# Kernel optimization log

Hardware: AMD Instinct MI355X
Metric: run time of the kernel (lower is better)

The kernel has to match this reference:

```python
import jax, jax.numpy as jnp
import numpy as np

# MX microscaling spec: block_size=32 shared power-of-2 scale, int8 elements (MXINT8),
# vector (SIMD) ops rounded to bfloat16 as in microxcaling's simd_* / vec_* ops.
BLOCK = 32
BITS = 8  # int8 element format: grid step 2^(shared_exp - (BITS-2)), range [-2^(BITS-1), 2^(BITS-1)-1]


def bf16_round(x):
    # bfloat=16 rounding used by simd_split / simd_add / vec ops
    return x.astype(jnp.bfloat16).astype(jnp.float32)


def mx_quant(x):
    """MXINT8 fake-quant along last (contraction) axis with block-shared exponent.
    Straight-through estimator for gradients."""
    s = x.shape
    xb = x.reshape(s[:-1] + (s[-1] // BLOCK, BLOCK))
    amax = jnp.max(jnp.abs(xb), axis=-1, keepdims=True)
    shared_exp = jnp.floor(jnp.log2(jnp.where(amax > 0, amax, 1.0)))
    scale = jnp.exp2(shared_exp - (BITS - 2))
    q = jnp.clip(jnp.round(xb / scale), -(2.0 ** (BITS - 1)), 2.0 ** (BITS - 1) - 1) * scale
    q = jnp.where(amax > 0, q, 0.0).reshape(s)
    return x + jax.lax.stop_gradient(q - x)


def mx_linear(x, W, b):
    # quantize activations and weights to MX blocks along K, fp32 accumulate, bf16 bias-add
    y = jnp.einsum('btk,ok->bto', mx_quant(x), mx_quant(W))
    return bf16_round(y + b)


def mx_layernorm(x, w, b, eps=1e-5):
    mu = jnp.mean(x, axis=-1, keepdims=True)
    var = jnp.mean(jnp.square(x - mu), axis=-1, keepdims=True)
    return bf16_round((x - mu) * jax.lax.rsqrt(var + eps) * w + b)


def mx_gelu(x):
    # tanh-approx gelu as in microxcaling, bf16-rounded output
    c = jnp.float32(0.7978845608028654)  # sqrt(2/pi)
    return bf16_round(0.5 * x * (1.0 + jnp.tanh(c * (x + 0.044715 * x * x * x))))


def setup_inputs() -> dict:
    key = jax.random.key(0)
    ks = jax.random.split(key, 5)
    B, S, H = 2, 2048, 2048
    inputs = jax.random.normal(ks[0], (B, S, H), dtype=jnp.float32)
    ln_w = jnp.ones((H,), dtype=jnp.float32)
    ln_b = jnp.zeros((H,), dtype=jnp.float32)
    W1 = jax.random.normal(ks[1], (4 * H, H), dtype=jnp.float32) * (1.0 / np.sqrt(H))
    b1 = jnp.zeros((4 * H,), dtype=jnp.float32)
    W2 = jax.random.normal(ks[2], (H, 4 * H), dtype=jnp.float32) * (1.0 / np.sqrt(4 * H))
    b2 = jnp.zeros((H,), dtype=jnp.float32)
    return {"inputs": inputs, "ln_w": ln_w, "ln_b": ln_b, "W1": W1, "b1": b1, "W2": W2, "b2": b2}


def reference(inputs, ln_w, ln_b, W1, b1, W2, b2):
    # simd_split: bf16-rounded copies for MLP branch and residual branch
    x = bf16_round(inputs)
    residual = bf16_round(inputs)
    h = mx_layernorm(x, ln_w, ln_b)
    h = mx_linear(h, W1, b1)          # [B,S,4H]
    h = mx_gelu(h)
    h = mx_linear(h, W2, b2)          # [B,S,H]
    return bf16_round(residual + h)    # simd_add
```

## Files before the change

### kernel.cpp

```cpp
#include <hip/hip_runtime.h>

#define DEVI __device__ __forceinline__

typedef __bf16 bf16x8 __attribute__((ext_vector_type(8)));
typedef float f32x4 __attribute__((ext_vector_type(4)));

DEVI unsigned short f2bf(float f) {
  unsigned u = __float_as_uint(f);
  u = (u + 0x7FFFu + ((u >> 16) & 1u)) >> 16;
  return (unsigned short)u;
}
DEVI float bf2f(unsigned short h) { return __uint_as_float(((unsigned)h) << 16); }
DEVI float bf16r(float f) { return bf2f(f2bf(f)); }

DEVI void mx_scales(float amax, float& scale, float& inv) {
  unsigned eb = __float_as_uint(amax) & 0x7f800000u;
  scale = __uint_as_float(eb - (6u << 23));
  inv   = __uint_as_float((260u << 23) - eb);
}

DEVI unsigned short quantv(float v, float scale, float inv) {
  float qv = rintf(v * inv);
  qv = fminf(fmaxf(qv, -128.f), 127.f);
  return f2bf(qv * scale);
}

DEVI void quant8(const float* h, float amax, unsigned short* q) {
  if (amax > 0.f) {
    float scale, inv;
    mx_scales(amax, scale, inv);
#pragma unroll
    for (int k = 0; k < 8; ++k) q[k] = quantv(h[k], scale, inv);
  } else {
#pragma unroll
    for (int k = 0; k < 8; ++k) q[k] = 0;
  }
}

template <int N>
DEVI float qmax_step(float x) {
  int y = __builtin_amdgcn_update_dpp(0, __float_as_int(x), 0x120 | N, 0xF, 0xF, true);
  return fmaxf(x, __int_as_float(y));
}
DEVI float quad_row_max(float x) {
  x = qmax_step<1>(x);
  x = qmax_step<2>(x);
  x = qmax_step<4>(x);
  x = qmax_step<8>(x);
  return x;
}

DEVI void gl2lds16(const void* g, void* l) {
  __builtin_amdgcn_global_load_lds(
      (__attribute__((address_space(1))) void*)const_cast<void*>(g),
      (__attribute__((address_space(3))) void*)l, 16, 0, 0);
}

DEVI uint4 pack8(const unsigned short* q) {
  uint4 o;
  o.x = (unsigned)q[0] | ((unsigned)q[1] << 16);
  o.y = (unsigned)q[2] | ((unsigned)q[3] << 16);
  o.z = (unsigned)q[4] | ((unsigned)q[5] << 16);
  o.w = (unsigned)q[6] | ((unsigned)q[7] << 16);
  return o;
}

__global__ __launch_bounds__(256) void prep_k(const float* __restrict__ W1,
                                              const float* __restrict__ W2,
                                              const float* __restrict__ X,
                                              const float* __restrict__ lw,
                                              const float* __restrict__ lb,
                                              unsigned short* __restrict__ qW1,
                                              unsigned short* __restrict__ qW2,
                                              unsigned short* __restrict__ a1) {
  __shared__ float red[4];
  const int bid = blockIdx.x;
  const int t = threadIdx.x;
  if (bid < 16384) {
    const float* src = (bid < 8192) ? W1 : W2;
    unsigned short* dst = (bid < 8192) ? qW1 : qW2;
    size_t idx = (size_t)(bid & 8191) * 256 + t;
    float4 v0 = ((const float4*)src)[idx * 2];
    float4 v1 = ((const float4*)src)[idx * 2 + 1];
    float h[8] = {v0.x, v0.y, v0.z, v0.w, v1.x, v1.y, v1.z, v1.w};
    float amax = 0.f;
#pragma unroll
    for (int k = 0; k < 8; ++k) amax = fmaxf(amax, fabsf(h[k]));
    amax = fmaxf(amax, __shfl_xor(amax, 1));
    amax = fmaxf(amax, __shfl_xor(amax, 2));
    unsigned short q[8];
    quant8(h, amax, q);
    ((uint4*)dst)[idx] = pack8(q);
  } else {
    const int H = 2048;
    const int row = bid - 16384;
    const int lane = t & 63, wave = t >> 6;
    const float* xr = X + (size_t)row * H;
    float4 v0 = ((const float4*)xr)[2 * t];
    float4 v1 = ((const float4*)xr)[2 * t + 1];
    float x[8] = {bf16r(v0.x), bf16r(v0.y), bf16r(v0.z), bf16r(v0.w),
                  bf16r(v1.x), bf16r(v1.y), bf16r(v1.z), bf16r(v1.w)};
    float s = 0.f;
#pragma unroll
    for (int k = 0; k < 8; ++k) s += x[k];
#pragma unroll
    for (int o = 32; o; o >>= 1) s += __shfl_xor(s, o);
    if (lane == 0) red[wave] = s;
    __syncthreads();
    float mu = (red[0] + red[1] + red[2] + red[3]) * (1.0f / H);
    __syncthreads();
    float v = 0.f;
#pragma unroll
    for (int k = 0; k < 8; ++k) { float d = x[k] - mu; v += d * d; }
#pragma unroll
    for (int o = 32; o; o >>= 1) v += __shfl_xor(v, o);
    if (lane == 0) red[wave] = v;
    __syncthreads();
    float var = (red[0] + red[1] + red[2] + red[3]) * (1.0f / H);
    float rstd = 1.0f / sqrtf(var + 1e-5f);
    float h[8];
    float amax = 0.f;
#pragma unroll
    for (int k = 0; k < 8; ++k) {
      int col = t * 8 + k;
      h[k] = bf16r((x[k] - mu) * rstd * lw[col] + lb[col]);
      amax = fmaxf(amax, fabsf(h[k]));
    }
    amax = fmaxf(amax, __shfl_xor(amax, 1));
    amax = fmaxf(amax, __shfl_xor(amax, 2));
    unsigned short q[8];
    quant8(h, amax, q);
    ((uint4*)(a1 + (size_t)row * H))[t] = pack8(q);
  }
}

template <int MODE>
__global__ __launch_bounds__(512, 2) void gemm_mx(const unsigned short* __restrict__ A,
                                                  const unsigned short* __restrict__ B,
                                                  int M, int N, int K,
                                                  const float* __restrict__ bias,
                                                  const float* __restrict__ resid,
                                                  void* __restrict__ outp) {
  __shared__ __align__(16) unsigned short As[3][128 * 64];
  __shared__ __align__(16) unsigned short Bs[3][256 * 64];

  const int tid = threadIdx.x;
  const int lane = tid & 63;
  const int wave = tid >> 6;
  const int lr = lane & 15;
  const int quad = lane >> 4;
  const int wr = (wave >> 2) * 64;
  const int wc = (wave & 3) * 64;

  const int m0 = blockIdx.y * 128;
  const int n0 = blockIdx.x * 256;

  const int chA = quad ^ (lr & 7);
  const int lroA = (wr + lr) * 64;
  const int lcoA = (wc + lr) * 64;

  const int sr8 = tid >> 3;
  const int sch = (tid & 7) ^ (sr8 & 7);
  size_t aoff[2], boff[4];
#pragma unroll
  for (int j = 0; j < 2; ++j) aoff[j] = (size_t)(m0 + j * 64 + sr8) * K + sch * 8;
#pragma unroll
  for (int j = 0; j < 4; ++j) boff[j] = (size_t)(n0 + j * 64 + sr8) * K + sch * 8;
  const int lb = (tid & ~63) * 8;

  const int NT = K >> 6;

  f32x4 acc[4][4];
#pragma unroll
  for (int i = 0; i < 4; ++i)
#pragma unroll
    for (int j = 0; j < 4; ++j) acc[i][j] = (f32x4){0.f, 0.f, 0.f, 0.f};

#pragma unroll
  for (int pt = 0; pt < 2; ++pt) {
    const size_t kadd = (size_t)pt * 64;
#pragma unroll
    for (int j = 0; j < 2; ++j) gl2lds16(A + aoff[j] + kadd, &As[pt][j * 4096 + lb]);
#pragma unroll
    for (int j = 0; j < 4; ++j) gl2lds16(B + boff[j] + kadd, &Bs[pt][j * 4096 + lb]);
  }
  asm volatile("s_waitcnt vmcnt(6)" ::: "memory");
  __builtin_amdgcn_s_barrier();

  int buf = 0;
  for (int t = 0; t < NT; ++t) {
    int nbuf = buf + 2; if (nbuf >= 3) nbuf -= 3;
    const bool pf = (t + 2) < NT;
    const size_t kadd = (size_t)(t + 2) * 64;

    {
      bf16x8 af[4], bfr[4];
      const unsigned short* Ap = &As[buf][lroA + chA * 8];
      const unsigned short* Bp = &Bs[buf][lcoA + chA * 8];
#pragma unroll
      for (int i = 0; i < 4; ++i) af[i] = *(const bf16x8*)(Ap + i * 1024);
#pragma unroll
      for (int j = 0; j < 4; ++j) bfr[j] = *(const bf16x8*)(Bp + j * 1024);
      if (pf) {
        gl2lds16(A + aoff[0] + kadd, &As[nbuf][lb]);
        gl2lds16(B + boff[0] + kadd, &Bs[nbuf][lb]);
        gl2lds16(B + boff[1] + kadd, &Bs[nbuf][4096 + lb]);
      }
      __builtin_amdgcn_s_barrier();
      asm volatile("s_waitcnt lgkmcnt(0)" ::: "memory");
      __builtin_amdgcn_sched_barrier(0);
      __builtin_amdgcn_s_setprio(1);
#pragma unroll
      for (int i = 0; i < 4; ++i)
#pragma unroll
        for (int j = 0; j < 4; ++j)
          acc[i][j] = __builtin_amdgcn_mfma_f32_16x16x32_bf16(af[i], bfr[j], acc[i][j], 0, 0, 0);
      __builtin_amdgcn_s_setprio(0);
      __builtin_amdgcn_s_barrier();
    }

    {
      bf16x8 af[4], bfr[4];
      const unsigned short* Ap = &As[buf][lroA + (chA ^ 4) * 8];
      const unsigned short* Bp = &Bs[buf][lcoA + (chA ^ 4) * 8];
#pragma unroll
      for (int i = 0; i < 4; ++i) af[i] = *(const bf16x8*)(Ap + i * 1024);
#pragma unroll
      for (int j = 0; j < 4; ++j) bfr[j] = *(const bf16x8*)(Bp + j * 1024);
      if (pf) {
        gl2lds16(A + aoff[1] + kadd, &As[nbuf][4096 + lb]);
        gl2lds16(B + boff[2] + kadd, &Bs[nbuf][8192 + lb]);
        gl2lds16(B + boff[3] + kadd, &Bs[nbuf][12288 + lb]);
      }
      __builtin_amdgcn_s_barrier();
      asm volatile("s_waitcnt lgkmcnt(0)" ::: "memory");
      __builtin_amdgcn_sched_barrier(0);
      __builtin_amdgcn_s_setprio(1);
#pragma unroll
      for (int i = 0; i < 4; ++i)
#pragma unroll
        for (int j = 0; j < 4; ++j)
          acc[i][j] = __builtin_amdgcn_mfma_f32_16x16x32_bf16(af[i], bfr[j], acc[i][j], 0, 0, 0);
      __builtin_amdgcn_s_setprio(0);
      if (pf) asm volatile("s_waitcnt vmcnt(6)" ::: "memory");
      else    asm volatile("s_waitcnt vmcnt(0)" ::: "memory");
      __builtin_amdgcn_s_barrier();
    }
    if (++buf == 3) buf = 0;
  }

  if (MODE == 1) {
#pragma unroll
    for (int i = 0; i < 4; ++i) {
#pragma unroll
      for (int r = 0; r < 4; ++r) {
        const int gm = m0 + wr + i * 16 + quad * 4 + r;
        float g[4];
#pragma unroll
        for (int j = 0; j < 4; ++j) {
          float tt = bf16r(acc[i][j][r] + bias[n0 + wc + j * 16 + lr]);
          float u = 0.7978845608028654f * (tt + 0.044715f * tt * tt * tt);
          g[j] = bf16r(0.5f * tt * (1.0f + tanhf(u)));
        }
        float a = quad_row_max(fmaxf(fabsf(g[0]), fabsf(g[1])));
        float b = quad_row_max(fmaxf(fabsf(g[2]), fabsf(g[3])));
        unsigned short q[4];
        if (a > 0.f) {
          float sc2, iv; mx_scales(a, sc2, iv);
          q[0] = quantv(g[0], sc2, iv); q[1] = quantv(g[1], sc2, iv);
        } else { q[0] = q[1] = 0; }
        if (b > 0.f) {
          float sc2, iv; mx_scales(b, sc2, iv);
          q[2] = quantv(g[2], sc2, iv); q[3] = quantv(g[3], sc2, iv);
        } else { q[2] = q[3] = 0; }
        unsigned short* orow = (unsigned short*)outp + (size_t)gm * N + n0 + wc + lr;
#pragma unroll
        for (int j = 0; j < 4; ++j) orow[j * 16] = q[j];
      }
    }
  } else {
#pragma unroll
    for (int i = 0; i < 4; ++i) {
#pragma unroll
      for (int j = 0; j < 4; ++j) {
#pragma unroll
        for (int r = 0; r < 4; ++r) {
          int gm = m0 + wr + i * 16 + quad * 4 + r;
          int gn = n0 + wc + j * 16 + lr;
          float h = bf16r(acc[i][j][r] + bias[gn]);
          float rr = bf16r(resid[(size_t)gm * N + gn]);
          ((float*)outp)[(size_t)gm * N + gn] = bf16r(rr + h);
        }
      }
    }
  }
  (void)M;
}

extern "C" void kernel_launch(void* const* d_in, const int* in_sizes, int n_in,
                              void* d_out, int out_size, void* d_ws, size_t ws_size,
                              hipStream_t stream) {
  const float* inputs = (const float*)d_in[0];
  const float* ln_w   = (const float*)d_in[1];
  const float* ln_b   = (const float*)d_in[2];
  const float* W1     = (const float*)d_in[3];
  const float* b1     = (const float*)d_in[4];
  const float* W2     = (const float*)d_in[5];
  const float* b2     = (const float*)d_in[6];
  float* out = (float*)d_out;
  char* ws = (char*)d_ws;
  (void)in_sizes; (void)n_in; (void)out_size; (void)ws_size;

  unsigned short* qW1  = (unsigned short*)(ws);
  unsigned short* qW2  = (unsigned short*)(ws + (size_t)33554432);
  unsigned short* a1   = (unsigned short*)(ws + (size_t)67108864);
  unsigned short* act2 = (unsigned short*)(ws + (size_t)83886080);

  const int M = 4096;

  prep_k<<<20480, 256, 0, stream>>>(W1, W2, inputs, ln_w, ln_b, qW1, qW2, a1);

  gemm_mx<1><<<dim3(8192 / 256, M / 128), 512, 0, stream>>>(
      a1, qW1, M, 8192, 2048, b1, nullptr, (void*)act2);

  gemm_mx<2><<<dim3(2048 / 256, M / 128), 512, 0, stream>>>(
      act2, qW2, M, 2048, 8192, b2, inputs, (void*)out);
}
```

Baseline: 513.4 us.

## Split GEMMs into specialized kernels with 256x256 tile and block swizzle for GEMM1

Replaces the templated GEMM with two specialized kernels that use compile-time sizes. The first GEMM moves to a 256x256 block tile with double buffering and 8x4 accumulators per wave, raising arithmetic intensity per LDS load. It reuses the B fragments across two A halves and adds a block-index swizzle for L2 locality. The second GEMM keeps its 128x256 triple-buffered pipeline but gains the swizzle and simplified loads, and the explicit lgkmcnt waits and sched barriers are dropped. The cost is more registers per wave and a smaller grid for GEMM1, which could hurt occupancy.

```diff
diff --git a/kernel.cpp b/kernel.cpp
--- a/kernel.cpp
+++ b/kernel.cpp
@@ -4,6 +4,8 @@
 
 typedef __bf16 bf16x8 __attribute__((ext_vector_type(8)));
 typedef float f32x4 __attribute__((ext_vector_type(4)));
+
+#define WAIT_VM(n) asm volatile("s_waitcnt vmcnt(" #n ")" ::: "memory")
 
 DEVI unsigned short f2bf(float f) {
   unsigned u = __float_as_uint(f);
@@ -134,41 +136,195 @@
   }
 }
 
-template <int MODE>
-__global__ __launch_bounds__(512, 2) void gemm_mx(const unsigned short* __restrict__ A,
+__global__ __launch_bounds__(512, 2) void gemm1_k(const unsigned short* __restrict__ A,
                                                   const unsigned short* __restrict__ B,
-                                                  int M, int N, int K,
+                                                  const float* __restrict__ bias,
+                                                  unsigned short* __restrict__ outp) {
+  constexpr int K = 2048, N = 8192, NT = K / 64;
+  __shared__ __align__(16) unsigned short As[2 * 256 * 64];
+  __shared__ __align__(16) unsigned short Bs[2 * 256 * 64];
+
+  const int tid = threadIdx.x;
+  const int lane = tid & 63;
+  const int lr = lane & 15;
+  const int quad = lane >> 4;
+  const int wave = tid >> 6;
+  const int wm = wave >> 2;
+  const int wn = wave & 3;
+
+  int lin = blockIdx.y * 32 + blockIdx.x;
+  lin = (lin & 7) * 64 + (lin >> 3);
+  const int m0 = (lin >> 5) * 256;
+  const int n0 = (lin & 31) * 256;
+
+  const int ch0 = quad ^ (lr & 7);
+  const int abase = (wm * 128 + lr) * 64;
+  const int bbase = (wn * 64 + lr) * 64;
+
+  const int srow = tid >> 3;
+  const int sch = (tid & 7) ^ (srow & 7);
+  const size_t aoff = (size_t)(m0 + srow) * K + sch * 8;
+  const size_t boff = (size_t)(n0 + srow) * K + sch * 8;
+  const int lb = (tid & ~63) * 8;
+
+  f32x4 acc[8][4];
+#pragma unroll
+  for (int i = 0; i < 8; ++i)
+#pragma unroll
+    for (int j = 0; j < 4; ++j) acc[i][j] = (f32x4){0.f, 0.f, 0.f, 0.f};
+
+#pragma unroll
+  for (int u = 0; u < 4; ++u) gl2lds16(B + boff + (size_t)u * 64 * K, Bs + u * 4096 + lb);
+  gl2lds16(A + aoff + (size_t)0 * 64 * K, As + 0 * 4096 + lb);
+  gl2lds16(A + aoff + (size_t)2 * 64 * K, As + 2 * 4096 + lb);
+  gl2lds16(A + aoff + (size_t)1 * 64 * K, As + 1 * 4096 + lb);
+  gl2lds16(A + aoff + (size_t)3 * 64 * K, As + 3 * 4096 + lb);
+  WAIT_VM(0);
+  __builtin_amdgcn_s_barrier();
+
+  for (int t = 0; t < NT; ++t) {
+    const int bb = (t & 1) * 16384;
+    const int nbb = ((t + 1) & 1) * 16384;
+    const bool pf = (t + 1) < NT;
+    const size_t kadd = (size_t)(t + 1) * 64;
+    const unsigned short* Ap = As + bb + abase;
+    const unsigned short* Bp = Bs + bb + bbase;
+    bf16x8 af[4], b0[4], b1[4];
+
+#pragma unroll
+    for (int i = 0; i < 4; ++i) af[i] = *(const bf16x8*)(Ap + ch0 * 8 + i * 1024);
+#pragma unroll
+    for (int j = 0; j < 4; ++j) b0[j] = *(const bf16x8*)(Bp + ch0 * 8 + j * 1024);
+    if (pf) {
+      gl2lds16(B + boff + kadd + (size_t)0 * 64 * K, Bs + nbb + 0 * 4096 + lb);
+      gl2lds16(B + boff + kadd + (size_t)1 * 64 * K, Bs + nbb + 1 * 4096 + lb);
+    }
+    __builtin_amdgcn_s_barrier();
+    __builtin_amdgcn_s_setprio(1);
+#pragma unroll
+    for (int i = 0; i < 4; ++i)
+#pragma unroll
+      for (int j = 0; j < 4; ++j)
+        acc[i][j] = __builtin_amdgcn_mfma_f32_16x16x32_bf16(af[i], b0[j], acc[i][j], 0, 0, 0);
+    __builtin_amdgcn_s_setprio(0);
+    __builtin_amdgcn_s_barrier();
+
+#pragma unroll
+    for (int i = 0; i < 4; ++i) af[i] = *(const bf16x8*)(Ap + (ch0 ^ 4) * 8 + i * 1024);
+#pragma unroll
+    for (int j = 0; j < 4; ++j) b1[j] = *(const bf16x8*)(Bp + (ch0 ^ 4) * 8 + j * 1024);
+    if (pf) {
+      gl2lds16(B + boff + kadd + (size_t)2 * 64 * K, Bs + nbb + 2 * 4096 + lb);
+      gl2lds16(B + boff + kadd + (size_t)3 * 64 * K, Bs + nbb + 3 * 4096 + lb);
+      WAIT_VM(4);
+    } else {
+      WAIT_VM(0);
+    }
+    __builtin_amdgcn_s_barrier();
+    __builtin_amdgcn_s_setprio(1);
+#pragma unroll
+    for (int i = 0; i < 4; ++i)
+#pragma unroll
+      for (int j = 0; j < 4; ++j)
+        acc[i][j] = __builtin_amdgcn_mfma_f32_16x16x32_bf16(af[i], b1[j], acc[i][j], 0, 0, 0);
+    __builtin_amdgcn_s_setprio(0);
+    __builtin_amdgcn_s_barrier();
+
+#pragma unroll
+    for (int i = 0; i < 4; ++i) af[i] = *(const bf16x8*)(Ap + 4096 + ch0 * 8 + i * 1024);
+    if (pf) {
+      gl2lds16(A + aoff + kadd + (size_t)0 * 64 * K, As + nbb + 0 * 4096 + lb);
+      gl2lds16(A + aoff + kadd + (size_t)2 * 64 * K, As + nbb + 2 * 4096 + lb);
+    }
+    __builtin_amdgcn_s_barrier();
+    __builtin_amdgcn_s_setprio(1);
+#pragma unroll
+    for (int i = 0; i < 4; ++i)
+#pragma unroll
+      for (int j = 0; j < 4; ++j)
+        acc[4 + i][j] = __builtin_amdgcn_mfma_f32_16x16x32_bf16(af[i], b0[j], acc[4 + i][j], 0, 0, 0);
+    __builtin_amdgcn_s_setprio(0);
+    __builtin_amdgcn_s_barrier();
+
+#pragma unroll
+    for (int i = 0; i < 4; ++i) af[i] = *(const bf16x8*)(Ap + 4096 + (ch0 ^ 4) * 8 + i * 1024);
+    if (pf) {
+      gl2lds16(A + aoff + kadd + (size_t)1 * 64 * K, As + nbb + 1 * 4096 + lb);
+      gl2lds16(A + aoff + kadd + (size_t)3 * 64 * K, As + nbb + 3 * 4096 + lb);
+      WAIT_VM(2);
+    }
+    __builtin_amdgcn_s_barrier();
+    __builtin_amdgcn_s_setprio(1);
+#pragma unroll
+    for (int i = 0; i < 4; ++i)
+#pragma unroll
+      for (int j = 0; j < 4; ++j)
+        acc[4 + i][j] = __builtin_amdgcn_mfma_f32_16x16x32_bf16(af[i], b1[j], acc[4 + i][j], 0, 0, 0);
+    __builtin_amdgcn_s_setprio(0);
+    __builtin_amdgcn_s_barrier();
+  }
+
+#pragma unroll
+  for (int i = 0; i < 8; ++i) {
+#pragma unroll
+    for (int r = 0; r < 4; ++r) {
+      const int gm = m0 + wm * 128 + i * 16 + quad * 4 + r;
+      float g[4];
+#pragma unroll
+      for (int j = 0; j < 4; ++j) {
+        float tt = bf16r(acc[i][j][r] + bias[n0 + wn * 64 + j * 16 + lr]);
+        float u = 0.7978845608028654f * (tt + 0.044715f * tt * tt * tt);
+        g[j] = bf16r(0.5f * tt * (1.0f + tanhf(u)));
+      }
+      float a = quad_row_max(fmaxf(fabsf(g[0]), fabsf(g[1])));
+      float b = quad_row_max(fmaxf(fabsf(g[2]), fabsf(g[3])));
+      unsigned short q[4];
+      if (a > 0.f) {
+        float sc2, iv; mx_scales(a, sc2, iv);
+        q[0] = quantv(g[0], sc2, iv); q[1] = quantv(g[1], sc2, iv);
+      } else { q[0] = q[1] = 0; }
+      if (b > 0.f) {
+        float sc2, iv; mx_scales(b, sc2, iv);
+        q[2] = quantv(g[2], sc2, iv); q[3] = quantv(g[3], sc2, iv);
+      } else { q[2] = q[3] = 0; }
+      unsigned short* orow = outp + (size_t)gm * N + n0 + wn * 64 + lr;
+#pragma unroll
+      for (int j = 0; j < 4; ++j) orow[j * 16] = q[j];
+    }
+  }
+}
+
+__global__ __launch_bounds__(512, 2) void gemm2_k(const unsigned short* __restrict__ A,
+                                                  const unsigned short* __restrict__ B,
                                                   const float* __restrict__ bias,
                                                   const float* __restrict__ resid,
-                                                  void* __restrict__ outp) {
-  __shared__ __align__(16) unsigned short As[3][128 * 64];
-  __shared__ __align__(16) unsigned short Bs[3][256 * 64];
+                                                  float* __restrict__ outp) {
+  constexpr int K = 8192, N = 2048, NT = K / 64;
+  __shared__ __align__(16) unsigned short As[3 * 128 * 64];
+  __shared__ __align__(16) unsigned short Bs[3 * 256 * 64];
 
   const int tid = threadIdx.x;
   const int lane = tid & 63;
-  const int wave = tid >> 6;
   const int lr = lane & 15;
   const int quad = lane >> 4;
-  const int wr = (wave >> 2) * 64;
-  const int wc = (wave & 3) * 64;
-
-  const int m0 = blockIdx.y * 128;
-  const int n0 = blockIdx.x * 256;
-
-  const int chA = quad ^ (lr & 7);
-  const int lroA = (wr + lr) * 64;
-  const int lcoA = (wc + lr) * 64;
-
-  const int sr8 = tid >> 3;
-  const int sch = (tid & 7) ^ (sr8 & 7);
-  size_t aoff[2], boff[4];
-#pragma unroll
-  for (int j = 0; j < 2; ++j) aoff[j] = (size_t)(m0 + j * 64 + sr8) * K + sch * 8;
-#pragma unroll
-  for (int j = 0; j < 4; ++j) boff[j] = (size_t)(n0 + j * 64 + sr8) * K + sch * 8;
+  const int wave = tid >> 6;
+  const int wm = wave >> 2;
+  const int wn = wave & 3;
+
+  int lin = blockIdx.y * 8 + blockIdx.x;
+  lin = (lin & 7) * 32 + (lin >> 3);
+  const int m0 = (lin >> 3) * 128;
+  const int n0 = (lin & 7) * 256;
+
+  const int ch0 = quad ^ (lr & 7);
+  const int abase = (wm * 64 + lr) * 64;
+  const int bbase = (wn * 64 + lr) * 64;
+
+  const int srow = tid >> 3;
+  const int sch = (tid & 7) ^ (srow & 7);
+  const size_t aoff = (size_t)(m0 + srow) * K + sch * 8;
+  const size_t boff = (size_t)(n0 + srow) * K + sch * 8;
   const int lb = (tid & ~63) * 8;
-
-  const int NT = K >> 6;
 
   f32x4 acc[4][4];
 #pragma unroll
@@ -180,121 +336,80 @@
   for (int pt = 0; pt < 2; ++pt) {
     const size_t kadd = (size_t)pt * 64;
 #pragma unroll
-    for (int j = 0; j < 2; ++j) gl2lds16(A + aoff[j] + kadd, &As[pt][j * 4096 + lb]);
-#pragma unroll
-    for (int j = 0; j < 4; ++j) gl2lds16(B + boff[j] + kadd, &Bs[pt][j * 4096 + lb]);
-  }
-  asm volatile("s_waitcnt vmcnt(6)" ::: "memory");
+    for (int u = 0; u < 4; ++u)
+      gl2lds16(B + boff + kadd + (size_t)u * 64 * K, Bs + pt * 16384 + u * 4096 + lb);
+    gl2lds16(A + aoff + kadd + (size_t)0 * 64 * K, As + pt * 8192 + 0 * 4096 + lb);
+    gl2lds16(A + aoff + kadd + (size_t)1 * 64 * K, As + pt * 8192 + 1 * 4096 + lb);
+  }
+  WAIT_VM(6);
   __builtin_amdgcn_s_barrier();
 
   int buf = 0;
   for (int t = 0; t < NT; ++t) {
-    int nbuf = buf + 2; if (nbuf >= 3) nbuf -= 3;
+    int nb = buf + 2; if (nb >= 3) nb -= 3;
     const bool pf = (t + 2) < NT;
     const size_t kadd = (size_t)(t + 2) * 64;
-
-    {
-      bf16x8 af[4], bfr[4];
-      const unsigned short* Ap = &As[buf][lroA + chA * 8];
-      const unsigned short* Bp = &Bs[buf][lcoA + chA * 8];
-#pragma unroll
-      for (int i = 0; i < 4; ++i) af[i] = *(const bf16x8*)(Ap + i * 1024);
-#pragma unroll
-      for (int j = 0; j < 4; ++j) bfr[j] = *(const bf16x8*)(Bp + j * 1024);
-      if (pf) {
-        gl2lds16(A + aoff[0] + kadd, &As[nbuf][lb]);
-        gl2lds16(B + boff[0] + kadd, &Bs[nbuf][lb]);
-        gl2lds16(B + boff[1] + kadd, &Bs[nbuf][4096 + lb]);
+    const unsigned short* Ap = As + buf * 8192 + abase;
+    const unsigned short* Bp = Bs + buf * 16384 + bbase;
+    bf16x8 af[4], bq[4];
+
+#pragma unroll
+    for (int i = 0; i < 4; ++i) af[i] = *(const bf16x8*)(Ap + ch0 * 8 + i * 1024);
+#pragma unroll
+    for (int j = 0; j < 4; ++j) bq[j] = *(const bf16x8*)(Bp + ch0 * 8 + j * 1024);
+    if (pf) {
+#pragma unroll
+      for (int u = 0; u < 4; ++u)
+        gl2lds16(B + boff + kadd + (size_t)u * 64 * K, Bs + nb * 16384 + u * 4096 + lb);
+    }
+    __builtin_amdgcn_s_barrier();
+    __builtin_amdgcn_s_setprio(1);
+#pragma unroll
+    for (int i = 0; i < 4; ++i)
+#pragma unroll
+      for (int j = 0; j < 4; ++j)
+        acc[i][j] = __builtin_amdgcn_mfma_f32_16x16x32_bf16(af[i], bq[j], acc[i][j], 0, 0, 0);
+    __builtin_amdgcn_s_setprio(0);
+    __builtin_amdgcn_s_barrier();
+
+#pragma unroll
+    for (int i = 0; i < 4; ++i) af[i] = *(const bf16x8*)(Ap + (ch0 ^ 4) * 8 + i * 1024);
+#pragma unroll
+    for (int j = 0; j < 4; ++j) bq[j] = *(const bf16x8*)(Bp + (ch0 ^ 4) * 8 + j * 1024);
+    if (pf) {
+      gl2lds16(A + aoff + kadd + (size_t)0 * 64 * K, As + nb * 8192 + 0 * 4096 + lb);
+      gl2lds16(A + aoff + kadd + (size_t)1 * 64 * K, As + nb * 8192 + 1 * 4096 + lb);
+      WAIT_VM(6);
+    } else if (t + 1 < NT) {
+      WAIT_VM(0);
+    }
+    __builtin_amdgcn_s_barrier();
+    __builtin_amdgcn_s_setprio(1);
+#pragma unroll
+    for (int i = 0; i < 4; ++i)
+#pragma unroll
+      for (int j = 0; j < 4; ++j)
+        acc[i][j] = __builtin_amdgcn_mfma_f32_16x16x32_bf16(af[i], bq[j], acc[i][j], 0, 0, 0);
+    __builtin_amdgcn_s_setprio(0);
+    __builtin_amdgcn_s_barrier();
+
+    if (++buf == 3) buf = 0;
+  }
+
+#pragma unroll
+  for (int i = 0; i < 4; ++i) {
+#pragma unroll
+    for (int j = 0; j < 4; ++j) {
+#pragma unroll
+      for (int r = 0; r < 4; ++r) {
+        int gm = m0 + wm * 64 + i * 16 + quad * 4 + r;
+        int gn = n0 + wn * 64 + j * 16 + lr;
+        float h = bf16r(acc[i][j][r] + bias[gn]);
+        float rr = bf16r(resid[(size_t)gm * N + gn]);
+        outp[(size_t)gm * N + gn] = bf16r(rr + h);
       }
-      __builtin_amdgcn_s_barrier();
-      asm volatile("s_waitcnt lgkmcnt(0)" ::: "memory");
-      __builtin_amdgcn_sched_barrier(0);
-      __builtin_amdgcn_s_setprio(1);
-#pragma unroll
-      for (int i = 0; i < 4; ++i)
-#pragma unroll
-        for (int j = 0; j < 4; ++j)
-          acc[i][j] = __builtin_amdgcn_mfma_f32_16x16x32_bf16(af[i], bfr[j], acc[i][j], 0, 0, 0);
-      __builtin_amdgcn_s_setprio(0);
-      __builtin_amdgcn_s_barrier();
-    }
-
-    {
-      bf16x8 af[4], bfr[4];
-      const unsigned short* Ap = &As[buf][lroA + (chA ^ 4) * 8];
-      const unsigned short* Bp = &Bs[buf][lcoA + (chA ^ 4) * 8];
-#pragma unroll
-      for (int i = 0; i < 4; ++i) af[i] = *(const bf16x8*)(Ap + i * 1024);
-#pragma unroll
-      for (int j = 0; j < 4; ++j) bfr[j] = *(const bf16x8*)(Bp + j * 1024);
-      if (pf) {
-        gl2lds16(A + aoff[1] + kadd, &As[nbuf][4096 + lb]);
-        gl2lds16(B + boff[2] + kadd, &Bs[nbuf][8192 + lb]);
-        gl2lds16(B + boff[3] + kadd, &Bs[nbuf][12288 + lb]);
-      }
-      __builtin_amdgcn_s_barrier();
-      asm volatile("s_waitcnt lgkmcnt(0)" ::: "memory");
-      __builtin_amdgcn_sched_barrier(0);
-      __builtin_amdgcn_s_setprio(1);
-#pragma unroll
-      for (int i = 0; i < 4; ++i)
-#pragma unroll
-        for (int j = 0; j < 4; ++j)
-          acc[i][j] = __builtin_amdgcn_mfma_f32_16x16x32_bf16(af[i], bfr[j], acc[i][j], 0, 0, 0);
-      __builtin_amdgcn_s_setprio(0);
-      if (pf) asm volatile("s_waitcnt vmcnt(6)" ::: "memory");
-      else    asm volatile("s_waitcnt vmcnt(0)" ::: "memory");
-      __builtin_amdgcn_s_barrier();
-    }
-    if (++buf == 3) buf = 0;
-  }
-
-  if (MODE == 1) {
-#pragma unroll
-    for (int i = 0; i < 4; ++i) {
-#pragma unroll
-      for (int r = 0; r < 4; ++r) {
-        const int gm = m0 + wr + i * 16 + quad * 4 + r;
-        float g[4];
-#pragma unroll
-        for (int j = 0; j < 4; ++j) {
-          float tt = bf16r(acc[i][j][r] + bias[n0 + wc + j * 16 + lr]);
-          float u = 0.7978845608028654f * (tt + 0.044715f * tt * tt * tt);
-          g[j] = bf16r(0.5f * tt * (1.0f + tanhf(u)));
-        }
-        float a = quad_row_max(fmaxf(fabsf(g[0]), fabsf(g[1])));
-        float b = quad_row_max(fmaxf(fabsf(g[2]), fabsf(g[3])));
-        unsigned short q[4];
-        if (a > 0.f) {
-          float sc2, iv; mx_scales(a, sc2, iv);
-          q[0] = quantv(g[0], sc2, iv); q[1] = quantv(g[1], sc2, iv);
-        } else { q[0] = q[1] = 0; }
-        if (b > 0.f) {
-          float sc2, iv; mx_scales(b, sc2, iv);
-          q[2] = quantv(g[2], sc2, iv); q[3] = quantv(g[3], sc2, iv);
-        } else { q[2] = q[3] = 0; }
-        unsigned short* orow = (unsigned short*)outp + (size_t)gm * N + n0 + wc + lr;
-#pragma unroll
-        for (int j = 0; j < 4; ++j) orow[j * 16] = q[j];
-      }
-    }
-  } else {
-#pragma unroll
-    for (int i = 0; i < 4; ++i) {
-#pragma unroll
-      for (int j = 0; j < 4; ++j) {
-#pragma unroll
-        for (int r = 0; r < 4; ++r) {
-          int gm = m0 + wr + i * 16 + quad * 4 + r;
-          int gn = n0 + wc + j * 16 + lr;
-          float h = bf16r(acc[i][j][r] + bias[gn]);
-          float rr = bf16r(resid[(size_t)gm * N + gn]);
-          ((float*)outp)[(size_t)gm * N + gn] = bf16r(rr + h);
-        }
-      }
-    }
-  }
-  (void)M;
+    }
+  }
 }
 
 extern "C" void kernel_launch(void* const* d_in, const int* in_sizes, int n_in,
@@ -316,13 +431,9 @@
   unsigned short* a1   = (unsigned short*)(ws + (size_t)67108864);
   unsigned short* act2 = (unsigned short*)(ws + (size_t)83886080);
 
-  const int M = 4096;
-
   prep_k<<<20480, 256, 0, stream>>>(W1, W2, inputs, ln_w, ln_b, qW1, qW2, a1);
 
-  gemm_mx<1><<<dim3(8192 / 256, M / 128), 512, 0, stream>>>(
-      a1, qW1, M, 8192, 2048, b1, nullptr, (void*)act2);
-
-  gemm_mx<2><<<dim3(2048 / 256, M / 128), 512, 0, stream>>>(
-      act2, qW2, M, 2048, 8192, b2, inputs, (void*)out);
-}
+  gemm1_k<<<dim3(8192 / 256, 4096 / 256), 512, 0, stream>>>(a1, qW1, b1, act2);
+
+  gemm2_k<<<dim3(2048 / 256, 4096 / 128), 512, 0, stream>>>(act2, qW2, b2, inputs, out);
+}
```

Measured after the change: 514.2 us. About the same (+0.2%).
